# Optimization experiments

Hardware: AMD Instinct MI355X
Metric: run time of the kernel (lower is better)

The kernel has to match this reference:

```python
import jax, jax.numpy as jnp
import numpy as np

H, E, DFF = 1024, 8, 4096


def setup_inputs() -> dict:
    key = jax.random.key(0)
    ks = jax.random.split(key, 7)
    s = lambda *shape: 1.0 / np.sqrt(shape[-2] if len(shape) > 1 else shape[-1])
    x = jax.random.normal(ks[0], (2, 2048, H), dtype=jnp.float32)
    Wr = jax.random.normal(ks[1], (H, E), dtype=jnp.float32) * (1.0 / np.sqrt(H))
    br = jnp.zeros((E,), dtype=jnp.float32)
    W1 = jax.random.normal(ks[2], (E, H, DFF), dtype=jnp.float32) * (1.0 / np.sqrt(H))
    b1 = jnp.zeros((E, DFF), dtype=jnp.float32)
    W2 = jax.random.normal(ks[3], (E, DFF, H), dtype=jnp.float32) * (1.0 / np.sqrt(DFF))
    b2 = jnp.zeros((E, H), dtype=jnp.float32)
    return {"x": x, "Wr": Wr, "br": br, "W1": W1, "b1": b1, "W2": W2, "b2": b2}


def reference(x, Wr, br, W1, b1, W2, b2):
    B, S, Hd = x.shape
    n_exp = W1.shape[0]
    xt = x.reshape(-1, Hd)                      # (T, H)
    logits = xt @ Wr + br                       # (T, E)
    probs = jax.nn.softmax(logits, axis=-1)
    gate = jnp.max(probs, axis=-1)              # (T,) top-1 gate value
    idx = jnp.argmax(probs, axis=-1)            # (T,) chosen expert
    # dense all-expert FFN, then one-hot combine (vectorized equivalent of per-token loop)
    h1 = jnp.maximum(jnp.einsum('th,ehf->etf', xt, W1) + b1[:, None, :], 0.0)  # (E,T,DFF)
    ye = jnp.einsum('etf,efh->eth', h1, W2) + b2[:, None, :]                   # (E,T,H)
    onehot = jax.nn.one_hot(idx, n_exp, dtype=xt.dtype)                        # (T,E)
    y = jnp.einsum('te,eth->th', onehot, ye) * gate[:, None]                   # (T,H)
    return y.reshape(B, S, Hd)
```

## Files before the change

### kernel.cpp

```cpp
#include <hip/hip_runtime.h>
#include <stdint.h>

typedef unsigned short u16;
typedef __attribute__((ext_vector_type(8))) short s16x8;
typedef __attribute__((ext_vector_type(4))) float f32x4;
typedef __attribute__((ext_vector_type(4))) unsigned uint4v;

#define NEXP 8
#define HD 1024
#define DFF 4096
#define BM 128
#define BN 128
#define BK 64

#define CT_S 136

__device__ __forceinline__ u16 f2bf(float f) {
  union { float f; unsigned u; } c; c.f = f;
  unsigned r = c.u + 0x7fffu + ((c.u >> 16) & 1u);
  return (u16)(r >> 16);
}

__device__ __forceinline__ unsigned cvtpk(float a, float b) {
  unsigned r;
  asm("v_cvt_pk_bf16_f32 %0, %1, %2" : "=v"(r) : "v"(a), "v"(b));
  return r;
}

__device__ __forceinline__ void gload_lds16(const void* g, const void* l) {
  __builtin_amdgcn_global_load_lds(
      (const __attribute__((address_space(1))) unsigned int*)(uintptr_t)g,
      (__attribute__((address_space(3))) unsigned int*)(unsigned)(uintptr_t)l,
      16, 0, 0);
}

__global__ __launch_bounds__(64) void zero_k(int* counts) {
  if (threadIdx.x < NEXP) counts[threadIdx.x] = 0;
}

template <int K, int N>
__device__ __forceinline__ void convt_tile(const float* __restrict__ W,
    u16* __restrict__ Wt, int idx, u16* __restrict__ T) {
  const int e = idx >> 9;
  const int ti = idx & 511;
  const int k0 = (ti % (K / 128)) * 128;
  const int n0 = (ti / (K / 128)) * 64;
  const float* src = W + (size_t)e * K * N;
  u16* dst = Wt + (size_t)e * K * N;
  const int t = threadIdx.x;
  const int m = t & 15, g = t >> 4;
  const int kq = g * 8, nq = m * 4;
  f32x4 v[8];
#pragma unroll
  for (int i = 0; i < 8; ++i)
    v[i] = *(const f32x4*)(src + (size_t)(k0 + kq + i) * N + n0 + nq);
#pragma unroll
  for (int j = 0; j < 4; ++j) {
    uint4v q;
    q[0] = cvtpk(v[0][j], v[1][j]);
    q[1] = cvtpk(v[2][j], v[3][j]);
    q[2] = cvtpk(v[4][j], v[5][j]);
    q[3] = cvtpk(v[6][j], v[7][j]);
    *(uint4v*)&T[(nq + j) * CT_S + kq] = q;
  }
  __syncthreads();
#pragma unroll
  for (int r = 0; r < 4; ++r) {
    const int nn = r * 16 + g;
    const int c8 = m * 8;
    uint4v q = *(const uint4v*)&T[nn * CT_S + c8];
    *(uint4v*)(dst + (size_t)(n0 + nn) * K + k0 + c8) = q;
  }
}

__global__ __launch_bounds__(256) void prep1_k(
    const float* __restrict__ x, const float* __restrict__ Wr,
    const float* __restrict__ br, int* __restrict__ counts,
    int* __restrict__ tok_exp, float* __restrict__ tok_gate,
    const float* __restrict__ W1, u16* __restrict__ W1t, int T) {
  __shared__ __align__(16) u16 Tt[64 * CT_S];
  const int bid = blockIdx.x;
  const int NBR = T / 4;
  if (bid >= NBR) {
    convt_tile<HD, DFF>(W1, W1t, bid - NBR, Tt);
    return;
  }
  const int w = threadIdx.x >> 6, l = threadIdx.x & 63;
  const int t = bid * 4 + w;
  const float4* xr = (const float4*)(x + (size_t)t * HD);
  float acc[NEXP];
#pragma unroll
  for (int j = 0; j < NEXP; ++j) acc[j] = 0.f;
#pragma unroll
  for (int i = 0; i < 4; ++i) {
    float4 v = xr[l + i * 64];
    const int h = (l + i * 64) * 4;
    const float* w0 = Wr + (size_t)h * NEXP;
#pragma unroll
    for (int c = 0; c < 4; ++c) {
      float xv = (c == 0) ? v.x : (c == 1) ? v.y : (c == 2) ? v.z : v.w;
      const float4* wr4 = (const float4*)(w0 + c * NEXP);
      float4 a = wr4[0], b = wr4[1];
      acc[0] += xv * a.x; acc[1] += xv * a.y; acc[2] += xv * a.z; acc[3] += xv * a.w;
      acc[4] += xv * b.x; acc[5] += xv * b.y; acc[6] += xv * b.z; acc[7] += xv * b.w;
    }
  }
#pragma unroll
  for (int j = 0; j < NEXP; ++j)
#pragma unroll
    for (int off = 32; off > 0; off >>= 1) acc[j] += __shfl_xor(acc[j], off);
  if (l == 0) {
    float lg[NEXP];
    float best = acc[0] + br[0]; int bi = 0;
    lg[0] = best;
#pragma unroll
    for (int j = 1; j < NEXP; ++j) {
      lg[j] = acc[j] + br[j];
      if (lg[j] > best) { best = lg[j]; bi = j; }
    }
    float s = 0.f;
#pragma unroll
    for (int j = 0; j < NEXP; ++j) s += expf(lg[j] - best);
    tok_exp[t] = bi;
    tok_gate[t] = 1.0f / s;
    atomicAdd(&counts[bi], 1);
  }
}

__global__ __launch_bounds__(64) void scan_k(const int* __restrict__ counts,
    int* __restrict__ seg, int* __restrict__ cursor,
    int* __restrict__ ntile, int* __restrict__ tile_e, int* __restrict__ tile_m) {
  if (threadIdx.x == 0) {
    int s = 0, nt = 0;
#pragma unroll
    for (int e = 0; e < NEXP; ++e) {
      seg[e] = s; cursor[e] = s;
      int c = counts[e];
      for (int m = 0; m < c; m += BM) { tile_e[nt] = e; tile_m[nt] = m; ++nt; }
      s += c;
    }
    seg[NEXP] = s;
    ntile[0] = nt;
  }
}

__global__ __launch_bounds__(256) void gather_k(const float* __restrict__ x,
    const int* __restrict__ tok_exp, const float* __restrict__ tok_gate,
    int* __restrict__ cursor, int* __restrict__ perm, float* __restrict__ gatep,
    u16* __restrict__ Xg) {
  const int w = threadIdx.x >> 6, l = threadIdx.x & 63;
  const int t = blockIdx.x * 4 + w;
  int pos = 0;
  if (l == 0) {
    int e = tok_exp[t];
    pos = atomicAdd(&cursor[e], 1);
    perm[pos] = t;
    gatep[pos] = tok_gate[t];
  }
  pos = __shfl(pos, 0);
  const float4* xr = (const float4*)(x + (size_t)t * HD);
  ushort4* dst = (ushort4*)(Xg + (size_t)pos * HD);
#pragma unroll
  for (int i = 0; i < HD / 4 / 64; ++i) {
    float4 v = xr[l + i * 64];
    ushort4 o;
    o.x = f2bf(v.x); o.y = f2bf(v.y); o.z = f2bf(v.z); o.w = f2bf(v.w);
    dst[l + i * 64] = o;
  }
}

template <int KD, int ND, int EPI, int KSPLIT>
__device__ __forceinline__ void gemm_body(
    u16* __restrict__ As, u16* __restrict__ Bs,
    const u16* __restrict__ A, const u16* __restrict__ Bt,
    const float* __restrict__ bias, const int* __restrict__ seg,
    const int* __restrict__ ntile, const int* __restrict__ tile_e,
    const int* __restrict__ tile_m,
    u16* __restrict__ H1out, float* __restrict__ Pt,
    int bx, int by, int ks) {
  if (by >= ntile[0]) return;
  const int e  = tile_e[by];
  const int m0 = tile_m[by];
  const int s0 = seg[e];
  const int cnt = seg[e + 1] - s0;
  const int n0 = bx * BN;
  constexpr int NT = (KD / KSPLIT) / BK;
  const int kbase = ks * (KD / KSPLIT);

  const int t = threadIdx.x;
  const int l = t & 63, w = t >> 6;
  const int wr = w >> 1, wc = w & 1;

  const f32x4 fzero = {0.f, 0.f, 0.f, 0.f};
  f32x4 acc[4][4];
#pragma unroll
  for (int i = 0; i < 4; ++i)
#pragma unroll
    for (int j = 0; j < 4; ++j) acc[i][j] = fzero;

  const int sub = t & 7, r8 = t >> 3;
  const int koff = (sub ^ (r8 & 7)) * 8;
  int aoff[4], boff[4];
  const u16* bte = Bt + (size_t)e * ND * KD;
#pragma unroll
  for (int c = 0; c < 4; ++c) {
    int row = c * 32 + r8;
    int rg = m0 + row; if (rg >= cnt) rg = cnt - 1;
    aoff[c] = (s0 + rg) * KD + kbase + koff;
    boff[c] = (n0 + row) * KD + kbase + koff;
  }

  for (int tt = 0; tt < NT; ++tt) {
    __syncthreads();
    const int ko = tt * BK;
#pragma unroll
    for (int c = 0; c < 4; ++c)
      gload_lds16(A + (size_t)aoff[c] + ko, &As[(c * 256 + t) * 8]);
#pragma unroll
    for (int c = 0; c < 4; ++c)
      gload_lds16(bte + (size_t)boff[c] + ko, &Bs[(c * 256 + t) * 8]);
    __syncthreads();
#pragma unroll
    for (int s = 0; s < 2; ++s) {
      const int fo = ((s * 4 + (l >> 4)) ^ (l & 7)) * 8;
      s16x8 af[4], bfr[4];
#pragma unroll
      for (int mi = 0; mi < 4; ++mi)
        af[mi] = *(const s16x8*)&As[(wr * 64 + mi * 16 + (l & 15)) * BK + fo];
#pragma unroll
      for (int ni = 0; ni < 4; ++ni)
        bfr[ni] = *(const s16x8*)&Bs[(wc * 64 + ni * 16 + (l & 15)) * BK + fo];
#pragma unroll
      for (int mi = 0; mi < 4; ++mi)
#pragma unroll
        for (int ni = 0; ni < 4; ++ni)
          acc[mi][ni] = __builtin_amdgcn_mfma_f32_16x16x32_bf16(af[mi], bfr[ni], acc[mi][ni], 0, 0, 0);
    }
  }

  const int lr = (l >> 4) * 4;
  const int lc = l & 15;

  if constexpr (EPI == 0) {
    float bv2[4];
#pragma unroll
    for (int ni = 0; ni < 4; ++ni)
      bv2[ni] = bias[(size_t)e * ND + n0 + wc * 64 + ni * 16 + lc];
#pragma unroll
    for (int mi = 0; mi < 4; ++mi) {
#pragma unroll
      for (int r = 0; r < 4; ++r) {
        int row = m0 + wr * 64 + mi * 16 + lr + r;
        if (row < cnt) {
          u16* hrow = H1out + (size_t)(s0 + row) * ND + n0 + wc * 64;
#pragma unroll
          for (int ni = 0; ni < 4; ++ni) {
            float v = acc[mi][ni][r] + bv2[ni];
            v = v > 0.f ? v : 0.f;
            hrow[ni * 16 + lc] = f2bf(v);
          }
        }
      }
    }
  } else {
    const int totT = seg[NEXP];
#pragma unroll
    for (int mi = 0; mi < 4; ++mi) {
#pragma unroll
      for (int r = 0; r < 4; ++r) {
        int row = m0 + wr * 64 + mi * 16 + lr + r;
        if (row < cnt) {
          float* prow = Pt + ((size_t)ks * totT + s0 + row) * ND + n0 + wc * 64;
#pragma unroll
          for (int ni = 0; ni < 4; ++ni)
            prow[ni * 16 + lc] = acc[mi][ni][r];
        }
      }
    }
  }
}

__global__ __launch_bounds__(256, 4) void gemm1_fused_k(
    const u16* __restrict__ Xg, const u16* __restrict__ W1t,
    const float* __restrict__ b1, const int* __restrict__ seg,
    const int* __restrict__ ntile, const int* __restrict__ tile_e,
    const int* __restrict__ tile_m, u16* __restrict__ H1,
    const float* __restrict__ W2, u16* __restrict__ W2t, int ng1) {
  __shared__ __align__(16) u16 sh[2 * BM * BK];
  const int bid = blockIdx.x;
  if (bid < ng1) {
    gemm_body<HD, DFF, 0, 1>(sh, sh + BM * BK, Xg, W1t, b1, seg, ntile, tile_e,
                             tile_m, H1, nullptr, bid % (DFF / BN), bid / (DFF / BN), 0);
  } else {
    convt_tile<DFF, HD>(W2, W2t, bid - ng1, sh);
  }
}

__global__ __launch_bounds__(256, 4) void gemm2_k(
    const u16* __restrict__ H1, const u16* __restrict__ W2t,
    const int* __restrict__ seg, const int* __restrict__ ntile,
    const int* __restrict__ tile_e, const int* __restrict__ tile_m,
    float* __restrict__ Pt) {
  __shared__ __align__(16) u16 sh[2 * BM * BK];
  gemm_body<DFF, HD, 2, 4>(sh, sh + BM * BK, H1, W2t, nullptr, seg, ntile, tile_e,
                           tile_m, nullptr, Pt, blockIdx.x, blockIdx.y, blockIdx.z);
}

__global__ __launch_bounds__(256) void reduce_k(const float* __restrict__ Pt,
    const float* __restrict__ b2, const int* __restrict__ perm,
    const float* __restrict__ gatep, const int* __restrict__ tok_exp,
    float* __restrict__ out) {
  const int pos = blockIdx.x;
  const int totT = gridDim.x;
  const int tok = perm[pos];
  const float g = gatep[pos];
  const int e = tok_exp[tok];
  const int h = threadIdx.x * 4;
  float4 s = *(const float4*)(Pt + ((size_t)0 * totT + pos) * HD + h);
#pragma unroll
  for (int k = 1; k < 4; ++k) {
    float4 p = *(const float4*)(Pt + ((size_t)k * totT + pos) * HD + h);
    s.x += p.x; s.y += p.y; s.z += p.z; s.w += p.w;
  }
  float4 b = *(const float4*)(b2 + (size_t)e * HD + h);
  float4 o;
  o.x = (s.x + b.x) * g; o.y = (s.y + b.y) * g;
  o.z = (s.z + b.z) * g; o.w = (s.w + b.w) * g;
  *(float4*)(out + (size_t)tok * HD + h) = o;
}

extern "C" void kernel_launch(void* const* d_in, const int* in_sizes, int n_in,
                              void* d_out, int out_size, void* d_ws, size_t ws_size,
                              hipStream_t stream) {
  const float* x  = (const float*)d_in[0];
  const float* Wr = (const float*)d_in[1];
  const float* br = (const float*)d_in[2];
  const float* W1 = (const float*)d_in[3];
  const float* b1 = (const float*)d_in[4];
  const float* W2 = (const float*)d_in[5];
  const float* b2 = (const float*)d_in[6];
  float* out = (float*)d_out;

  const int T = in_sizes[0] / HD;
  char* ws = (char*)d_ws;
  int*   counts   = (int*)(ws + 0);
  int*   cursor   = (int*)(ws + 64);
  int*   seg      = (int*)(ws + 128);
  int*   ntile    = (int*)(ws + 192);
  int*   tile_e   = (int*)(ws + 256);
  int*   tile_m   = (int*)(ws + 512);
  int*   tok_exp  = (int*)(ws + 1024);
  float* tok_gate = (float*)(ws + 1024 + 4 * (size_t)T);
  int*   perm     = (int*)(ws + 1024 + 8 * (size_t)T);
  float* gatep    = (float*)(ws + 1024 + 12 * (size_t)T);
  u16*   Xg       = (u16*)(ws + 1024 + 16 * (size_t)T);
  u16*   H1       = (u16*)(ws + 1024 + 16 * (size_t)T + 2 * (size_t)T * HD);
  size_t off2     = 1024 + 16 * (size_t)T + 2 * (size_t)T * HD + 2 * (size_t)T * DFF;
  u16*   W1t      = (u16*)(ws + off2);
  u16*   W2t      = (u16*)(ws + off2 + 2 * (size_t)NEXP * HD * DFF);
  float* Pt       = (float*)W1t;

  hipLaunchKernelGGL(zero_k, dim3(1), dim3(64), 0, stream, counts);
  const int NBR = T / 4;
  const int NCT = 512 * NEXP;
  hipLaunchKernelGGL(prep1_k, dim3(NBR + NCT), dim3(256), 0, stream,
                     x, Wr, br, counts, tok_exp, tok_gate, W1, W1t, T);
  hipLaunchKernelGGL(scan_k, dim3(1), dim3(64), 0, stream, counts, seg, cursor, ntile, tile_e, tile_m);
  hipLaunchKernelGGL(gather_k, dim3(T / 4), dim3(256), 0, stream,
                     x, tok_exp, tok_gate, cursor, perm, gatep, Xg);
  const int maxtile = (T + BM - 1) / BM + NEXP - 1;
  const int ng1 = (DFF / BN) * maxtile;
  hipLaunchKernelGGL(gemm1_fused_k, dim3(ng1 + NCT), dim3(256), 0, stream,
                     Xg, W1t, b1, seg, ntile, tile_e, tile_m, H1, W2, W2t, ng1);
  hipLaunchKernelGGL(gemm2_k, dim3(HD / BN, maxtile, 4), dim3(256), 0, stream,
                     H1, W2t, seg, ntile, tile_e, tile_m, Pt);
  hipLaunchKernelGGL(reduce_k, dim3(T), dim3(256), 0, stream, Pt, b2, perm, gatep, tok_exp, out);
}
```

Measured before the change: 297.2 us.

## Drop LDS from weight transpose, persist converter blocks, pre-convert x to bf16

The fp32-to-bf16 weight transpose no longer stages through shared memory. Each thread reads 16 consecutive k rows for one column and writes one contiguous 32-byte chunk, and a fixed pool of blocks loops over several tiles. The conversion blocks are placed first in the grid so they launch ahead of the router and GEMM1 work. The router kernel also writes a bf16 copy of x into the H1 buffer, so the gather kernel copies half the bytes. The tradeoff is that loads are now scalar 4-byte per lane, coalesced across a wavefront, and each thread's 32-byte store hits a different 2 KB/8 KB-strided row.

```diff
diff --git a/kernel.cpp b/kernel.cpp
--- a/kernel.cpp
+++ b/kernel.cpp
@@ -12,8 +12,7 @@
 #define BM 128
 #define BN 128
 #define BK 64
-
-#define CT_S 136
+#define NPC 2048
 
 __device__ __forceinline__ u16 f2bf(float f) {
   union { float f; unsigned u; } c; c.f = f;
@@ -40,53 +39,46 @@
 
 template <int K, int N>
 __device__ __forceinline__ void convt_tile(const float* __restrict__ W,
-    u16* __restrict__ Wt, int idx, u16* __restrict__ T) {
-  const int e = idx >> 9;
-  const int ti = idx & 511;
-  const int k0 = (ti % (K / 128)) * 128;
-  const int n0 = (ti / (K / 128)) * 64;
-  const float* src = W + (size_t)e * K * N;
-  u16* dst = Wt + (size_t)e * K * N;
-  const int t = threadIdx.x;
-  const int m = t & 15, g = t >> 4;
-  const int kq = g * 8, nq = m * 4;
-  f32x4 v[8];
-#pragma unroll
-  for (int i = 0; i < 8; ++i)
-    v[i] = *(const f32x4*)(src + (size_t)(k0 + kq + i) * N + n0 + nq);
+                                           u16* __restrict__ Wt, int idx) {
+  constexpr int TPE = (K / 64) * (N / 64);
+  const int e = idx / TPE;
+  const int ti = idx % TPE;
+  const int k0 = (ti % (K / 64)) * 64;
+  const int n0 = (ti / (K / 64)) * 64;
+  const float* src = W + (size_t)e * K * N + (size_t)k0 * N + n0;
+  const int n = threadIdx.x & 63;
+  const int g = threadIdx.x >> 6;
+  float v[16];
+#pragma unroll
+  for (int i = 0; i < 16; ++i)
+    v[i] = src[(size_t)(g * 16 + i) * N + n];
+  uint4v q0, q1;
 #pragma unroll
   for (int j = 0; j < 4; ++j) {
-    uint4v q;
-    q[0] = cvtpk(v[0][j], v[1][j]);
-    q[1] = cvtpk(v[2][j], v[3][j]);
-    q[2] = cvtpk(v[4][j], v[5][j]);
-    q[3] = cvtpk(v[6][j], v[7][j]);
-    *(uint4v*)&T[(nq + j) * CT_S + kq] = q;
-  }
-  __syncthreads();
-#pragma unroll
-  for (int r = 0; r < 4; ++r) {
-    const int nn = r * 16 + g;
-    const int c8 = m * 8;
-    uint4v q = *(const uint4v*)&T[nn * CT_S + c8];
-    *(uint4v*)(dst + (size_t)(n0 + nn) * K + k0 + c8) = q;
-  }
+    q0[j] = cvtpk(v[2 * j], v[2 * j + 1]);
+    q1[j] = cvtpk(v[8 + 2 * j], v[9 + 2 * j]);
+  }
+  u16* d = Wt + (size_t)e * K * N + (size_t)(n0 + n) * K + k0 + g * 16;
+  *(uint4v*)d = q0;
+  *(uint4v*)(d + 8) = q1;
 }
 
 __global__ __launch_bounds__(256) void prep1_k(
     const float* __restrict__ x, const float* __restrict__ Wr,
     const float* __restrict__ br, int* __restrict__ counts,
     int* __restrict__ tok_exp, float* __restrict__ tok_gate,
-    const float* __restrict__ W1, u16* __restrict__ W1t, int T) {
-  __shared__ __align__(16) u16 Tt[64 * CT_S];
+    const float* __restrict__ W1, u16* __restrict__ W1t,
+    u16* __restrict__ Xbf, int T) {
   const int bid = blockIdx.x;
-  const int NBR = T / 4;
-  if (bid >= NBR) {
-    convt_tile<HD, DFF>(W1, W1t, bid - NBR, Tt);
+  if (bid < NPC) {
+    constexpr int NTL = NEXP * (HD / 64) * (DFF / 64);
+#pragma unroll
+    for (int i = 0; i < NTL / NPC; ++i)
+      convt_tile<HD, DFF>(W1, W1t, bid + i * NPC);
     return;
   }
   const int w = threadIdx.x >> 6, l = threadIdx.x & 63;
-  const int t = bid * 4 + w;
+  const int t = (bid - NPC) * 4 + w;
   const float4* xr = (const float4*)(x + (size_t)t * HD);
   float acc[NEXP];
 #pragma unroll
@@ -94,6 +86,8 @@
 #pragma unroll
   for (int i = 0; i < 4; ++i) {
     float4 v = xr[l + i * 64];
+    unsigned pa = cvtpk(v.x, v.y), pb = cvtpk(v.z, v.w);
+    *(uint2*)&Xbf[(size_t)t * HD + (l + i * 64) * 4] = make_uint2(pa, pb);
     const int h = (l + i * 64) * 4;
     const float* w0 = Wr + (size_t)h * NEXP;
 #pragma unroll
@@ -144,7 +138,7 @@
   }
 }
 
-__global__ __launch_bounds__(256) void gather_k(const float* __restrict__ x,
+__global__ __launch_bounds__(256) void gather_k(const u16* __restrict__ Xbf,
     const int* __restrict__ tok_exp, const float* __restrict__ tok_gate,
     int* __restrict__ cursor, int* __restrict__ perm, float* __restrict__ gatep,
     u16* __restrict__ Xg) {
@@ -158,15 +152,11 @@
     gatep[pos] = tok_gate[t];
   }
   pos = __shfl(pos, 0);
-  const float4* xr = (const float4*)(x + (size_t)t * HD);
-  ushort4* dst = (ushort4*)(Xg + (size_t)pos * HD);
-#pragma unroll
-  for (int i = 0; i < HD / 4 / 64; ++i) {
-    float4 v = xr[l + i * 64];
-    ushort4 o;
-    o.x = f2bf(v.x); o.y = f2bf(v.y); o.z = f2bf(v.z); o.w = f2bf(v.w);
-    dst[l + i * 64] = o;
-  }
+  const s16x8* srcr = (const s16x8*)(Xbf + (size_t)t * HD);
+  s16x8* dst = (s16x8*)(Xg + (size_t)pos * HD);
+#pragma unroll
+  for (int i = 0; i < HD / 8 / 64; ++i)
+    dst[l + i * 64] = srcr[l + i * 64];
 }
 
 template <int KD, int ND, int EPI, int KSPLIT>
@@ -285,14 +275,18 @@
     const float* __restrict__ b1, const int* __restrict__ seg,
     const int* __restrict__ ntile, const int* __restrict__ tile_e,
     const int* __restrict__ tile_m, u16* __restrict__ H1,
-    const float* __restrict__ W2, u16* __restrict__ W2t, int ng1) {
+    const float* __restrict__ W2, u16* __restrict__ W2t) {
   __shared__ __align__(16) u16 sh[2 * BM * BK];
   const int bid = blockIdx.x;
-  if (bid < ng1) {
+  if (bid < NPC) {
+    constexpr int NTL = NEXP * (DFF / 64) * (HD / 64);
+#pragma unroll
+    for (int i = 0; i < NTL / NPC; ++i)
+      convt_tile<DFF, HD>(W2, W2t, bid + i * NPC);
+  } else {
+    const int g = bid - NPC;
     gemm_body<HD, DFF, 0, 1>(sh, sh + BM * BK, Xg, W1t, b1, seg, ntile, tile_e,
-                             tile_m, H1, nullptr, bid % (DFF / BN), bid / (DFF / BN), 0);
-  } else {
-    convt_tile<DFF, HD>(W2, W2t, bid - ng1, sh);
+                             tile_m, H1, nullptr, g % (DFF / BN), g / (DFF / BN), 0);
   }
 }
 
@@ -359,19 +353,18 @@
   u16*   W1t      = (u16*)(ws + off2);
   u16*   W2t      = (u16*)(ws + off2 + 2 * (size_t)NEXP * HD * DFF);
   float* Pt       = (float*)W1t;
+  u16*   Xbf      = H1;
 
   hipLaunchKernelGGL(zero_k, dim3(1), dim3(64), 0, stream, counts);
-  const int NBR = T / 4;
-  const int NCT = 512 * NEXP;
-  hipLaunchKernelGGL(prep1_k, dim3(NBR + NCT), dim3(256), 0, stream,
-                     x, Wr, br, counts, tok_exp, tok_gate, W1, W1t, T);
+  hipLaunchKernelGGL(prep1_k, dim3(NPC + T / 4), dim3(256), 0, stream,
+                     x, Wr, br, counts, tok_exp, tok_gate, W1, W1t, Xbf, T);
   hipLaunchKernelGGL(scan_k, dim3(1), dim3(64), 0, stream, counts, seg, cursor, ntile, tile_e, tile_m);
   hipLaunchKernelGGL(gather_k, dim3(T / 4), dim3(256), 0, stream,
-                     x, tok_exp, tok_gate, cursor, perm, gatep, Xg);
+                     Xbf, tok_exp, tok_gate, cursor, perm, gatep, Xg);
   const int maxtile = (T + BM - 1) / BM + NEXP - 1;
   const int ng1 = (DFF / BN) * maxtile;
-  hipLaunchKernelGGL(gemm1_fused_k, dim3(ng1 + NCT), dim3(256), 0, stream,
-                     Xg, W1t, b1, seg, ntile, tile_e, tile_m, H1, W2, W2t, ng1);
+  hipLaunchKernelGGL(gemm1_fused_k, dim3(NPC + ng1), dim3(256), 0, stream,
+                     Xg, W1t, b1, seg, ntile, tile_e, tile_m, H1, W2, W2t);
   hipLaunchKernelGGL(gemm2_k, dim3(HD / BN, maxtile, 4), dim3(256), 0, stream,
                      H1, W2t, seg, ntile, tile_e, tile_m, Pt);
   hipLaunchKernelGGL(reduce_k, dim3(T), dim3(256), 0, stream, Pt, b2, perm, gatep, tok_exp, out);
```

New measurement: 359.7 us. 1.21x slower.

## Double-buffer LDS in grouped GEMMs and pre-convert x to bf16 in router

Applied to the files above, without the earlier changes.

The GEMM main loop now uses two LDS buffers, prefetching the next K tile with async global-to-LDS loads while MFMAs run on the current one, which drops one barrier per iteration. LDS per block doubles and launch bounds fall from 4 to 2 blocks per CU, trading occupancy for overlap. Separately, the router kernel writes a bf16 copy of x into the H1 scratch area, so the gather kernel copies half the bytes and skips the conversion.

```diff
diff --git a/kernel.cpp b/kernel.cpp
--- a/kernel.cpp
+++ b/kernel.cpp
@@ -14,6 +14,7 @@
 #define BK 64
 
 #define CT_S 136
+#define TILE_U16 (BM * BK)
 
 __device__ __forceinline__ u16 f2bf(float f) {
   union { float f; unsigned u; } c; c.f = f;
@@ -77,7 +78,8 @@
     const float* __restrict__ x, const float* __restrict__ Wr,
     const float* __restrict__ br, int* __restrict__ counts,
     int* __restrict__ tok_exp, float* __restrict__ tok_gate,
-    const float* __restrict__ W1, u16* __restrict__ W1t, int T) {
+    const float* __restrict__ W1, u16* __restrict__ W1t,
+    u16* __restrict__ Xbf, int T) {
   __shared__ __align__(16) u16 Tt[64 * CT_S];
   const int bid = blockIdx.x;
   const int NBR = T / 4;
@@ -94,6 +96,8 @@
 #pragma unroll
   for (int i = 0; i < 4; ++i) {
     float4 v = xr[l + i * 64];
+    unsigned pa = cvtpk(v.x, v.y), pb = cvtpk(v.z, v.w);
+    *(uint2*)&Xbf[(size_t)t * HD + (l + i * 64) * 4] = make_uint2(pa, pb);
     const int h = (l + i * 64) * 4;
     const float* w0 = Wr + (size_t)h * NEXP;
 #pragma unroll
@@ -144,7 +148,7 @@
   }
 }
 
-__global__ __launch_bounds__(256) void gather_k(const float* __restrict__ x,
+__global__ __launch_bounds__(256) void gather_k(const u16* __restrict__ Xbf,
     const int* __restrict__ tok_exp, const float* __restrict__ tok_gate,
     int* __restrict__ cursor, int* __restrict__ perm, float* __restrict__ gatep,
     u16* __restrict__ Xg) {
@@ -158,20 +162,16 @@
     gatep[pos] = tok_gate[t];
   }
   pos = __shfl(pos, 0);
-  const float4* xr = (const float4*)(x + (size_t)t * HD);
-  ushort4* dst = (ushort4*)(Xg + (size_t)pos * HD);
-#pragma unroll
-  for (int i = 0; i < HD / 4 / 64; ++i) {
-    float4 v = xr[l + i * 64];
-    ushort4 o;
-    o.x = f2bf(v.x); o.y = f2bf(v.y); o.z = f2bf(v.z); o.w = f2bf(v.w);
-    dst[l + i * 64] = o;
-  }
+  const s16x8* srcr = (const s16x8*)(Xbf + (size_t)t * HD);
+  s16x8* dst = (s16x8*)(Xg + (size_t)pos * HD);
+#pragma unroll
+  for (int i = 0; i < HD / 8 / 64; ++i)
+    dst[l + i * 64] = srcr[l + i * 64];
 }
 
 template <int KD, int ND, int EPI, int KSPLIT>
 __device__ __forceinline__ void gemm_body(
-    u16* __restrict__ As, u16* __restrict__ Bs,
+    u16* __restrict__ sh,
     const u16* __restrict__ A, const u16* __restrict__ Bt,
     const float* __restrict__ bias, const int* __restrict__ seg,
     const int* __restrict__ ntile, const int* __restrict__ tile_e,
@@ -210,33 +210,48 @@
     boff[c] = (n0 + row) * KD + kbase + koff;
   }
 
+  u16* Ac = sh;
+  u16* Bc = sh + TILE_U16;
+  u16* An = sh + 2 * TILE_U16;
+  u16* Bn = sh + 3 * TILE_U16;
+
+#define STAGE(pa, pb, tt) do { \
+    const int ko_ = (tt) * BK; \
+    _Pragma("unroll") for (int c_ = 0; c_ < 4; ++c_) \
+      gload_lds16(A + (size_t)aoff[c_] + ko_, (pa) + (c_ * 256 + t) * 8); \
+    _Pragma("unroll") for (int c_ = 0; c_ < 4; ++c_) \
+      gload_lds16(bte + (size_t)boff[c_] + ko_, (pb) + (c_ * 256 + t) * 8); \
+  } while (0)
+
+#define COMPUTE(pa, pb) do { \
+    _Pragma("unroll") for (int s_ = 0; s_ < 2; ++s_) { \
+      const int fo_ = ((s_ * 4 + (l >> 4)) ^ (l & 7)) * 8; \
+      s16x8 af_[4], bf_[4]; \
+      _Pragma("unroll") for (int mi_ = 0; mi_ < 4; ++mi_) \
+        af_[mi_] = *(const s16x8*)&(pa)[(wr * 64 + mi_ * 16 + (l & 15)) * BK + fo_]; \
+      _Pragma("unroll") for (int ni_ = 0; ni_ < 4; ++ni_) \
+        bf_[ni_] = *(const s16x8*)&(pb)[(wc * 64 + ni_ * 16 + (l & 15)) * BK + fo_]; \
+      _Pragma("unroll") for (int mi_ = 0; mi_ < 4; ++mi_) \
+        _Pragma("unroll") for (int ni_ = 0; ni_ < 4; ++ni_) \
+          acc[mi_][ni_] = __builtin_amdgcn_mfma_f32_16x16x32_bf16(af_[mi_], bf_[ni_], acc[mi_][ni_], 0, 0, 0); \
+    } \
+  } while (0)
+
+  STAGE(Ac, Bc, 0);
+  __syncthreads();
   for (int tt = 0; tt < NT; ++tt) {
-    __syncthreads();
-    const int ko = tt * BK;
-#pragma unroll
-    for (int c = 0; c < 4; ++c)
-      gload_lds16(A + (size_t)aoff[c] + ko, &As[(c * 256 + t) * 8]);
-#pragma unroll
-    for (int c = 0; c < 4; ++c)
-      gload_lds16(bte + (size_t)boff[c] + ko, &Bs[(c * 256 + t) * 8]);
-    __syncthreads();
-#pragma unroll
-    for (int s = 0; s < 2; ++s) {
-      const int fo = ((s * 4 + (l >> 4)) ^ (l & 7)) * 8;
-      s16x8 af[4], bfr[4];
-#pragma unroll
-      for (int mi = 0; mi < 4; ++mi)
-        af[mi] = *(const s16x8*)&As[(wr * 64 + mi * 16 + (l & 15)) * BK + fo];
-#pragma unroll
-      for (int ni = 0; ni < 4; ++ni)
-        bfr[ni] = *(const s16x8*)&Bs[(wc * 64 + ni * 16 + (l & 15)) * BK + fo];
-#pragma unroll
-      for (int mi = 0; mi < 4; ++mi)
-#pragma unroll
-        for (int ni = 0; ni < 4; ++ni)
-          acc[mi][ni] = __builtin_amdgcn_mfma_f32_16x16x32_bf16(af[mi], bfr[ni], acc[mi][ni], 0, 0, 0);
-    }
-  }
+    if (tt + 1 < NT) STAGE(An, Bn, tt + 1);
+    COMPUTE(Ac, Bc);
+    if (tt + 1 < NT) {
+      __syncthreads();
+      u16* x;
+      x = Ac; Ac = An; An = x;
+      x = Bc; Bc = Bn; Bn = x;
+    }
+  }
+
+#undef STAGE
+#undef COMPUTE
 
   const int lr = (l >> 4) * 4;
   const int lc = l & 15;
@@ -280,29 +295,29 @@
   }
 }
 
-__global__ __launch_bounds__(256, 4) void gemm1_fused_k(
+__global__ __launch_bounds__(256, 2) void gemm1_fused_k(
     const u16* __restrict__ Xg, const u16* __restrict__ W1t,
     const float* __restrict__ b1, const int* __restrict__ seg,
     const int* __restrict__ ntile, const int* __restrict__ tile_e,
     const int* __restrict__ tile_m, u16* __restrict__ H1,
     const float* __restrict__ W2, u16* __restrict__ W2t, int ng1) {
-  __shared__ __align__(16) u16 sh[2 * BM * BK];
+  __shared__ __align__(16) u16 sh[4 * TILE_U16];
   const int bid = blockIdx.x;
   if (bid < ng1) {
-    gemm_body<HD, DFF, 0, 1>(sh, sh + BM * BK, Xg, W1t, b1, seg, ntile, tile_e,
+    gemm_body<HD, DFF, 0, 1>(sh, Xg, W1t, b1, seg, ntile, tile_e,
                              tile_m, H1, nullptr, bid % (DFF / BN), bid / (DFF / BN), 0);
   } else {
     convt_tile<DFF, HD>(W2, W2t, bid - ng1, sh);
   }
 }
 
-__global__ __launch_bounds__(256, 4) void gemm2_k(
+__global__ __launch_bounds__(256, 2) void gemm2_k(
     const u16* __restrict__ H1, const u16* __restrict__ W2t,
     const int* __restrict__ seg, const int* __restrict__ ntile,
     const int* __restrict__ tile_e, const int* __restrict__ tile_m,
     float* __restrict__ Pt) {
-  __shared__ __align__(16) u16 sh[2 * BM * BK];
-  gemm_body<DFF, HD, 2, 4>(sh, sh + BM * BK, H1, W2t, nullptr, seg, ntile, tile_e,
+  __shared__ __align__(16) u16 sh[4 * TILE_U16];
+  gemm_body<DFF, HD, 2, 4>(sh, H1, W2t, nullptr, seg, ntile, tile_e,
                            tile_m, nullptr, Pt, blockIdx.x, blockIdx.y, blockIdx.z);
 }
 
@@ -359,15 +374,16 @@
   u16*   W1t      = (u16*)(ws + off2);
   u16*   W2t      = (u16*)(ws + off2 + 2 * (size_t)NEXP * HD * DFF);
   float* Pt       = (float*)W1t;
+  u16*   Xbf      = H1;
 
   hipLaunchKernelGGL(zero_k, dim3(1), dim3(64), 0, stream, counts);
   const int NBR = T / 4;
   const int NCT = 512 * NEXP;
   hipLaunchKernelGGL(prep1_k, dim3(NBR + NCT), dim3(256), 0, stream,
-                     x, Wr, br, counts, tok_exp, tok_gate, W1, W1t, T);
+                     x, Wr, br, counts, tok_exp, tok_gate, W1, W1t, Xbf, T);
   hipLaunchKernelGGL(scan_k, dim3(1), dim3(64), 0, stream, counts, seg, cursor, ntile, tile_e, tile_m);
   hipLaunchKernelGGL(gather_k, dim3(T / 4), dim3(256), 0, stream,
-                     x, tok_exp, tok_gate, cursor, perm, gatep, Xg);
+                     Xbf, tok_exp, tok_gate, cursor, perm, gatep, Xg);
   const int maxtile = (T + BM - 1) / BM + NEXP - 1;
   const int ng1 = (DFF / BN) * maxtile;
   hipLaunchKernelGGL(gemm1_fused_k, dim3(ng1 + NCT), dim3(256), 0, stream,
```

Measured after the change: 298.7 us. Within noise of the previous version (+0.5%).
